# Kernel tuning notes

Hardware: AMD Instinct MI355X
Metric: run time of the kernel (lower is better)

## Reference

```python
import jax, jax.numpy as jnp
import numpy as np

DIM = 128; NH = 4; WS = 7; SS = 3
ZP, HP, WP = 14, 56, 56
NMLP = 512; EPS = 1e-5
N = WS ** 3  # tokens per window (343)


def _ln(x, g, b):
    m = x.mean(-1, keepdims=True)
    v = x.var(-1, keepdims=True)
    return (x - m) / jnp.sqrt(v + EPS) * g + b


def _rel_index():
    # static relative-position index for a cubic (WS,WS,WS) window
    c = np.stack(np.meshgrid(np.arange(WS), np.arange(WS), np.arange(WS), indexing='ij')).reshape(3, -1)
    rel = (c[:, :, None] - c[:, None, :]).transpose(1, 2, 0) + (WS - 1)
    rel[..., 0] *= (2 * WS - 1) ** 2
    rel[..., 1] *= (2 * WS - 1)
    return rel.sum(-1).reshape(-1)  # [N*N]


def _attn_mask():
    # static shifted-window attention mask, [nW, N, N]
    img = np.zeros((ZP, HP, WP), np.float32)
    cnt = 0
    sl = (slice(0, -WS), slice(-WS, -SS), slice(-SS, None))
    for z in sl:
        for h in sl:
            for w in sl:
                img[z, h, w] = cnt
                cnt += 1
    m = img.reshape(ZP // WS, WS, HP // WS, WS, WP // WS, WS)
    m = m.transpose(0, 2, 4, 1, 3, 5).reshape(-1, N)
    d = m[:, None, :] - m[:, :, None]
    return np.where(d != 0, np.float32(-100.0), np.float32(0.0))


_REL_IDX = jnp.asarray(_rel_index())
_MASK = jnp.asarray(_attn_mask())


def setup_inputs() -> dict:
    key = jax.random.key(0)
    ks = jax.random.split(key, 8)
    return {
        'x': jax.random.normal(ks[0], (2, ZP, HP, WP, DIM), jnp.float32),
        'norm1_g': jnp.ones((DIM,), jnp.float32),
        'norm1_b': jnp.zeros((DIM,), jnp.float32),
        'qkv_w': jax.random.normal(ks[1], (DIM, 3 * DIM), jnp.float32) * 0.02,
        'qkv_b': jnp.zeros((3 * DIM,), jnp.float32),
        'rel_table': jax.random.normal(ks[2], ((2 * WS - 1) ** 3, NH), jnp.float32) * 0.02,
        'proj_w': jax.random.normal(ks[3], (DIM, DIM), jnp.float32) * 0.02,
        'proj_b': jnp.zeros((DIM,), jnp.float32),
        'norm2_g': jnp.ones((DIM,), jnp.float32),
        'norm2_b': jnp.zeros((DIM,), jnp.float32),
        'fc1_w': jax.random.normal(ks[4], (DIM, NMLP), jnp.float32) * 0.02,
        'fc1_b': jnp.zeros((NMLP,), jnp.float32),
        'fc2_w': jax.random.normal(ks[5], (NMLP, DIM), jnp.float32) * 0.02,
        'fc2_b': jnp.zeros((DIM,), jnp.float32),
    }


def reference(x, norm1_g, norm1_b, qkv_w, qkv_b, rel_table, proj_w, proj_b,
              norm2_g, norm2_b, fc1_w, fc1_b, fc2_w, fc2_b):
    B, Z, H, W, C = x.shape
    hd = C // NH
    scale = hd ** -0.5
    shortcut = x
    xn = _ln(x, norm1_g, norm1_b)
    # cyclic shift
    xs = jnp.roll(xn, (-SS, -SS, -SS), axis=(1, 2, 3))
    # window partition -> [B*nW, N, C]
    xw = xs.reshape(B, Z // WS, WS, H // WS, WS, W // WS, WS, C)
    xw = xw.transpose(0, 1, 3, 5, 2, 4, 6, 7).reshape(-1, N, C)
    qkv = (xw @ qkv_w + qkv_b).reshape(-1, N, 3, NH, hd).transpose(2, 0, 3, 1, 4)
    q, k, v = qkv[0], qkv[1], qkv[2]  # [Bn, NH, N, hd]
    attn = jnp.einsum('bhnd,bhmd->bhnm', q * scale, k)
    bias = rel_table[_REL_IDX].reshape(N, N, NH).transpose(2, 0, 1)  # [NH, N, N]
    attn = attn + bias[None]
    nW = _MASK.shape[0]
    attn = attn.reshape(B, nW, NH, N, N) + _MASK[None, :, None]
    attn = jax.nn.softmax(attn.reshape(-1, NH, N, N), axis=-1)
    out = jnp.einsum('bhnm,bhmd->bhnd', attn, v)
    out = out.transpose(0, 2, 1, 3).reshape(-1, N, C)
    out = out @ proj_w + proj_b
    # window reverse -> [B, Z, H, W, C]
    out = out.reshape(B, Z // WS, H // WS, W // WS, WS, WS, WS, C)
    out = out.transpose(0, 1, 4, 2, 5, 3, 6, 7).reshape(B, Z, H, W, C)
    out = jnp.roll(out, (SS, SS, SS), axis=(1, 2, 3))
    x1 = shortcut + out
    y = _ln(x1, norm2_g, norm2_b)
    y = jax.nn.gelu(y @ fc1_w + fc1_b, approximate=False) @ fc2_w + fc2_b
    return x1 + y
```

## Files before the change

### kernel.cpp

```cpp
#include <hip/hip_runtime.h>


typedef __attribute__((ext_vector_type(8))) _Float16 half8;
typedef __attribute__((ext_vector_type(4))) _Float16 half4;
typedef __attribute__((ext_vector_type(4))) float floatx4;

#define DEV static __device__ __forceinline__

DEV floatx4 MFMA(half8 a, half8 b, floatx4 c) {
  return __builtin_amdgcn_mfma_f32_16x16x32_f16(a, b, c, 0, 0, 0);
}

DEV float gelu_f(float v) {
  return v / (1.f + __expf(-1.702f * v));
}

DEV void f4arr(float4 v, float o[4]) {
  o[0] = v.x; o[1] = v.y; o[2] = v.z; o[3] = v.w;
}

DEV void stage_load(half8 pf[8], const _Float16* src, int rst, int tid) {
#pragma unroll
  for (int it = 0; it < 8; ++it) {
    int e = it * 256 + tid;
    int row = e >> 4, seg = e & 15;
    pf[it] = *(const half8*)&src[(size_t)row * rst + seg * 8];
  }
}
DEV void stage_store(_Float16* wb, const half8 pf[8], int tid) {
#pragma unroll
  for (int it = 0; it < 8; ++it) {
    int e = it * 256 + tid;
    int row = e >> 4, seg = e & 15;
    *(half8*)&wb[row * 136 + seg * 8] = pf[it];
  }
}
DEV void stage_tile(_Float16* wb, const _Float16* src, int rst, int tid) {
  half8 pf[8];
  stage_load(pf, src, rst, tid);
  stage_store(wb, pf, tid);
}

__global__ __launch_bounds__(256) void k_prep(
    const float* __restrict__ rel, _Float16* __restrict__ biasH,
    const float* __restrict__ w1, const float* __restrict__ w2,
    const float* __restrict__ wq, const float* __restrict__ wp,
    _Float16* __restrict__ w1h, _Float16* __restrict__ w2h,
    _Float16* __restrict__ wqh, _Float16* __restrict__ wph) {
  int gid = blockIdx.x * 256 + threadIdx.x;
  if (gid < 495616) {
    int reg = gid & 3, ml = (gid >> 2) & 15;
    int t = gid >> 6;
    int rb = t % 88; t /= 88;
    int nt = t % 22; int h = t / 22;
    int row = rb * 4 + reg, col = nt * 16 + ml;
    float val = -30000.f;
    if (row < 343 && col < 343) {
      int lzi = row / 49, ri = row - lzi * 49, lhi = ri / 7, lwi = ri - lhi * 7;
      int lzj = col / 49, rj = col - lzj * 49, lhj = rj / 7, lwj = rj - lhj * 7;
      int idx = (lzi - lzj + 6) * 169 + (lhi - lhj + 6) * 13 + (lwi - lwj + 6);
      val = rel[idx * 4 + h];
    }
    biasH[gid] = (_Float16)val;
    return;
  }
  int i = gid - 495616;
  if (i < 65536) {
    int n = i >> 7, k = i & 127;
    w1h[i] = (_Float16)w1[k * 512 + n];
  } else if (i < 131072) {
    int j = i - 65536; int n = j >> 9, k = j & 511;
    w2h[j] = (_Float16)w2[k * 128 + n];
  } else if (i < 180224) {
    int j = i - 131072; int n = j >> 7, k = j & 127;
    wqh[j] = (_Float16)wq[k * 384 + n];
  } else if (i < 196608) {
    int j = i - 180224; int n = j >> 7, k = j & 127;
    wph[j] = (_Float16)wp[k * 128 + n];
  }
}

__global__ __launch_bounds__(256) void k_ln_qkv(
    const float* __restrict__ x, const float* __restrict__ g1,
    const float* __restrict__ b1, const _Float16* __restrict__ wqh,
    const float* __restrict__ bq, _Float16* __restrict__ qkv) {
  __shared__ __align__(16) _Float16 wb[128 * 136];
  const int tid = threadIdx.x, lane = tid & 63, wid = tid >> 6;
  const int ml = lane & 15, quad = lane >> 4;
  const int task = blockIdx.x * 4 + wid;
  const int w = task / 11, pr = task - (task / 11) * 11;
  const int b_ = w >> 7, r = w & 127;
  const int wz = r >> 6, wh = (r >> 3) & 7, ww = r & 7;

  half8 a0[4], a1[4];
#pragma unroll
  for (int hf = 0; hf < 2; ++hf) {
    int t = pr * 32 + hf * 16 + ml; if (t > 342) t = 342;
    int lz = t / 49, rr = t - lz * 49, lh = rr / 7, lw = rr - lh * 7;
    int oz = wz * 7 + lz + 3; if (oz >= 14) oz -= 14;
    int oh = wh * 7 + lh + 3; if (oh >= 56) oh -= 56;
    int ow = ww * 7 + lw + 3; if (ow >= 56) ow -= 56;
    const float* xp = x + ((((b_ * 14 + oz) * 56 + oh) * 56 + ow) << 7);
    float xv[32];
    float s = 0.f, ss = 0.f;
#pragma unroll
    for (int ks = 0; ks < 4; ++ks) {
      float4 p0 = *(const float4*)(xp + ks * 32 + quad * 8);
      float4 p1 = *(const float4*)(xp + ks * 32 + quad * 8 + 4);
      xv[ks * 8 + 0] = p0.x; xv[ks * 8 + 1] = p0.y; xv[ks * 8 + 2] = p0.z; xv[ks * 8 + 3] = p0.w;
      xv[ks * 8 + 4] = p1.x; xv[ks * 8 + 5] = p1.y; xv[ks * 8 + 6] = p1.z; xv[ks * 8 + 7] = p1.w;
      s += (p0.x + p0.y) + (p0.z + p0.w) + (p1.x + p1.y) + (p1.z + p1.w);
      ss += (p0.x * p0.x + p0.y * p0.y) + (p0.z * p0.z + p0.w * p0.w) +
            (p1.x * p1.x + p1.y * p1.y) + (p1.z * p1.z + p1.w * p1.w);
    }
    s += __shfl_xor(s, 16); s += __shfl_xor(s, 32);
    ss += __shfl_xor(ss, 16); ss += __shfl_xor(ss, 32);
    float mean = s * 0.0078125f;
    float rstd = rsqrtf(ss * 0.0078125f - mean * mean + 1e-5f);
#pragma unroll
    for (int ks = 0; ks < 4; ++ks) {
      int k0 = ks * 32 + quad * 8;
      float4 gg0 = *(const float4*)(g1 + k0), gg1 = *(const float4*)(g1 + k0 + 4);
      float4 bb0 = *(const float4*)(b1 + k0), bb1 = *(const float4*)(b1 + k0 + 4);
      half8 a;
      a[0] = (_Float16)((xv[ks * 8 + 0] - mean) * rstd * gg0.x + bb0.x);
      a[1] = (_Float16)((xv[ks * 8 + 1] - mean) * rstd * gg0.y + bb0.y);
      a[2] = (_Float16)((xv[ks * 8 + 2] - mean) * rstd * gg0.z + bb0.z);
      a[3] = (_Float16)((xv[ks * 8 + 3] - mean) * rstd * gg0.w + bb0.w);
      a[4] = (_Float16)((xv[ks * 8 + 4] - mean) * rstd * gg1.x + bb1.x);
      a[5] = (_Float16)((xv[ks * 8 + 5] - mean) * rstd * gg1.y + bb1.y);
      a[6] = (_Float16)((xv[ks * 8 + 6] - mean) * rstd * gg1.z + bb1.z);
      a[7] = (_Float16)((xv[ks * 8 + 7] - mean) * rstd * gg1.w + bb1.w);
      if (hf == 0) a0[ks] = a; else a1[ks] = a;
    }
  }

  const int t0 = pr * 32 + ml;
  const int t1 = t0 + 16;
  _Float16* q0 = qkv + ((size_t)w * 343 + t0) * 384;
  _Float16* q1 = qkv + ((size_t)w * 343 + (t1 < 343 ? t1 : 342)) * 384;

  for (int c = 0; c < 3; ++c) {
    __syncthreads();
    stage_tile(wb, wqh + (size_t)c * 128 * 128, 128, tid);
    __syncthreads();
    for (int ntl = 0; ntl < 8; ++ntl) {
      floatx4 acc0 = {0.f, 0.f, 0.f, 0.f}, acc1 = {0.f, 0.f, 0.f, 0.f};
#pragma unroll
      for (int ks = 0; ks < 4; ++ks) {
        half8 bb = *(const half8*)&wb[(ntl * 16 + ml) * 136 + ks * 32 + quad * 8];
        acc0 = MFMA(bb, a0[ks], acc0);
        acc1 = MFMA(bb, a1[ks], acc1);
      }
      const int colb = c * 128 + ntl * 16 + quad * 4;
      float qb[4]; f4arr(*(const float4*)&bq[colb], qb);
      half4 s0, s1;
#pragma unroll
      for (int reg = 0; reg < 4; ++reg) {
        s0[reg] = (_Float16)(acc0[reg] + qb[reg]);
        s1[reg] = (_Float16)(acc1[reg] + qb[reg]);
      }
      *(half4*)&q0[colb] = s0;
      if (t1 < 343) *(half4*)&q1[colb] = s1;
    }
  }
}

__global__ __launch_bounds__(512, 2) void k_attn(const _Float16* __restrict__ qkv,
                                                 const _Float16* __restrict__ biasH,
                                                 _Float16* __restrict__ aout) {
  __shared__ __align__(16) _Float16 kl[352 * 40];
  __shared__ __align__(16) _Float16 vt[32 * 360];
  __shared__ __align__(16) _Float16 P[8][16 * 360];
  __shared__ float sums[8][16];
  __shared__ unsigned char region[352];
  const int tid = threadIdx.x;
  const int w = blockIdx.x >> 2, head = blockIdx.x & 3;
  const int r = w & 127;
  const int wz = r >> 6, wh = (r >> 3) & 7, ww = r & 7;
  const bool fz = (wz == 1), fh = (wh == 7), fw = (ww == 7);

  for (int t = tid; t < 352; t += 512) {
    int rg = 255;
    if (t < 343) {
      int lz = t / 49, rr = t - lz * 49, lh = rr / 7, lw = rr - lh * 7;
      int rz = fz ? (lz < 4 ? 1 : 2) : 0;
      int rh2 = fh ? (lh < 4 ? 1 : 2) : 0;
      int rw2 = fw ? (lw < 4 ? 1 : 2) : 0;
      rg = rz * 9 + rh2 * 3 + rw2;
    }
    region[t] = (unsigned char)rg;
  }
  const _Float16* qkvw = qkv + (size_t)w * 343 * 384;
  for (int e = tid; e < 352 * 4; e += 512) {
    int t = e >> 2, d8 = (e & 3) * 8;
    half8 v;
    if (t < 343) {
      v = *(const half8*)&qkvw[t * 384 + 128 + head * 32 + d8];
    } else {
#pragma unroll
      for (int j = 0; j < 8; ++j) v[j] = (_Float16)0.f;
    }
    *(half8*)&kl[t * 40 + d8] = v;
  }
  for (int e = tid; e < 343 * 4; e += 512) {
    int t = e >> 2, d8 = (e & 3) * 8;
    half8 v = *(const half8*)&qkvw[t * 384 + 256 + head * 32 + d8];
#pragma unroll
    for (int j = 0; j < 8; ++j) vt[(d8 + j) * 360 + t] = v[j];
  }
  for (int e = tid; e < 9 * 32; e += 512) {
    int t = 343 + (e >> 5), d = e & 31;
    vt[d * 360 + t] = (_Float16)0.f;
  }
  __syncthreads();

  const int lane = tid & 63, wid = tid >> 6;
  const int ml = lane & 15, quad = lane >> 4;
  _Float16* Pw = &P[wid][0];
  const float scale = 0.17677669529663687f;

  for (int rt = wid; rt < 22; rt += 8) {
    const int row0 = rt * 16;
    int qrow = row0 + ml; if (qrow > 342) qrow = 342;
    half8 aq = *(const half8*)&qkvw[qrow * 384 + head * 32 + quad * 8];
    floatx4 S[22];
#pragma unroll
    for (int nt = 0; nt < 22; ++nt) {
      half8 bk = *(const half8*)&kl[(nt * 16 + ml) * 40 + quad * 8];
      S[nt] = MFMA(aq, bk, (floatx4){0.f, 0.f, 0.f, 0.f});
    }
    int rrow[4];
#pragma unroll
    for (int reg = 0; reg < 4; ++reg) rrow[reg] = region[row0 + quad * 4 + reg];
    const int rb = rt * 4 + quad;
    float sm[4] = {0.f, 0.f, 0.f, 0.f};
#pragma unroll
    for (int nt = 0; nt < 22; ++nt) {
      half4 b4 = *(const half4*)&biasH[((((head * 22 + nt) * 88 + rb) << 4) + ml) * 4];
      int rc = region[nt * 16 + ml];
#pragma unroll
      for (int reg = 0; reg < 4; ++reg) {
        float v = fmaf(S[nt][reg], scale, (float)b4[reg]);
        if (rc != rrow[reg]) v = -30000.f;
        float e = __expf(v);
        sm[reg] += e;
        Pw[(quad * 4 + reg) * 360 + nt * 16 + ml] = (_Float16)e;
      }
    }
#pragma unroll
    for (int d = 1; d < 16; d <<= 1)
#pragma unroll
      for (int reg = 0; reg < 4; ++reg) sm[reg] += __shfl_xor(sm[reg], d, 16);
    if (ml == 0) {
#pragma unroll
      for (int reg = 0; reg < 4; ++reg) sums[wid][quad * 4 + reg] = sm[reg];
    }
    floatx4 o0 = {0.f, 0.f, 0.f, 0.f}, o1 = {0.f, 0.f, 0.f, 0.f};
#pragma unroll
    for (int ks = 0; ks < 11; ++ks) {
      half8 bp = *(const half8*)&Pw[ml * 360 + ks * 32 + quad * 8];
      half8 a0 = *(const half8*)&vt[ml * 360 + ks * 32 + quad * 8];
      half8 a1 = *(const half8*)&vt[(16 + ml) * 360 + ks * 32 + quad * 8];
      o0 = MFMA(a0, bp, o0);
      o1 = MFMA(a1, bp, o1);
    }
    const int orow = row0 + ml;
    if (orow < 343) {
      float inv = 1.f / sums[wid][ml];
      _Float16* op = aout + ((size_t)w * 343 + orow) * 128 + head * 32;
      half4 s0, s1;
#pragma unroll
      for (int reg = 0; reg < 4; ++reg) {
        s0[reg] = (_Float16)(o0[reg] * inv);
        s1[reg] = (_Float16)(o1[reg] * inv);
      }
      *(half4*)&op[quad * 4] = s0;
      *(half4*)&op[16 + quad * 4] = s1;
    }
  }
}

__global__ __launch_bounds__(256, 2) void k_pm(
    const _Float16* __restrict__ aout, const _Float16* __restrict__ wph,
    const float* __restrict__ bp, const float* __restrict__ x,
    const float* __restrict__ g2, const float* __restrict__ nb2,
    const _Float16* __restrict__ w1h, const float* __restrict__ bfc1,
    const _Float16* __restrict__ w2h, const float* __restrict__ bfc2,
    float* __restrict__ out) {
  __shared__ __align__(16) _Float16 hc[4][32 * 136];
  __shared__ __align__(16) _Float16 wb[128 * 136];
  const int tid = threadIdx.x, lane = tid & 63, wid = tid >> 6;
  const int ml = lane & 15, quad = lane >> 4;
  const int task = blockIdx.x * 4 + wid;
  const int w = task / 11, pr = task - (task / 11) * 11;
  const int b_ = w >> 7, r = w & 127;
  const int wz = r >> 6, wh = (r >> 3) & 7, ww = r & 7;
  const _Float16* ap = aout + (size_t)w * 343 * 128;
  _Float16* hw = &hc[wid][0];

  half8 pf[8];
  stage_load(pf, wph, 128, tid);

  int ra = pr * 32 + ml; if (ra > 342) ra = 342;
  int rbm = pr * 32 + 16 + ml; if (rbm > 342) rbm = 342;
  half8 a0[4], a1[4];
#pragma unroll
  for (int ks = 0; ks < 4; ++ks) {
    a0[ks] = *(const half8*)&ap[ra * 128 + ks * 32 + quad * 8];
    a1[ks] = *(const half8*)&ap[rbm * 128 + ks * 32 + quad * 8];
  }
  int tok[2];
#pragma unroll
  for (int mt = 0; mt < 2; ++mt) {
    int t = pr * 32 + mt * 16 + ml;
    if (t < 343) {
      int lz = t / 49, rr = t - lz * 49, lh = rr / 7, lw = rr - lh * 7;
      int oz = wz * 7 + lz + 3; if (oz >= 14) oz -= 14;
      int oh = wh * 7 + lh + 3; if (oh >= 56) oh -= 56;
      int ow = ww * 7 + lw + 3; if (ow >= 56) ow -= 56;
      tok[mt] = ((b_ * 14 + oz) * 56 + oh) * 56 + ow;
    } else {
      tok[mt] = -1;
    }
  }
  stage_store(wb, pf, tid);
  __syncthreads();
  stage_load(pf, w1h, 128, tid);

  floatx4 px[8][2];
  for (int nt = 0; nt < 8; ++nt) {
    floatx4 acc0 = {0.f, 0.f, 0.f, 0.f}, acc1 = {0.f, 0.f, 0.f, 0.f};
#pragma unroll
    for (int ks = 0; ks < 4; ++ks) {
      half8 bb = *(const half8*)&wb[(nt * 16 + ml) * 136 + ks * 32 + quad * 8];
      acc0 = MFMA(bb, a0[ks], acc0);
      acc1 = MFMA(bb, a1[ks], acc1);
    }
    const int colb = nt * 16 + quad * 4;
    float pb4[4]; f4arr(*(const float4*)&bp[colb], pb4);
    float xr0[4] = {0.f, 0.f, 0.f, 0.f}, xr1[4] = {0.f, 0.f, 0.f, 0.f};
    if (tok[0] >= 0) f4arr(*(const float4*)&x[(size_t)tok[0] * 128 + colb], xr0);
    if (tok[1] >= 0) f4arr(*(const float4*)&x[(size_t)tok[1] * 128 + colb], xr1);
#pragma unroll
    for (int reg = 0; reg < 4; ++reg) {
      px[nt][0][reg] = acc0[reg] + pb4[reg] + xr0[reg];
      px[nt][1][reg] = acc1[reg] + pb4[reg] + xr1[reg];
    }
  }

  float mean[2], rstd[2];
#pragma unroll
  for (int mt = 0; mt < 2; ++mt) {
    float s = 0.f, ss = 0.f;
#pragma unroll
    for (int nt = 0; nt < 8; ++nt)
#pragma unroll
      for (int reg = 0; reg < 4; ++reg) {
        float v = px[nt][mt][reg];
        s += v; ss += v * v;
      }
    s += __shfl_xor(s, 16); s += __shfl_xor(s, 32);
    ss += __shfl_xor(ss, 16); ss += __shfl_xor(ss, 32);
    float m = s * 0.0078125f;
    mean[mt] = m;
    rstd[mt] = rsqrtf(ss * 0.0078125f - m * m + 1e-5f);
  }

  for (int nt = 0; nt < 8; ++nt) {
    const int colb = nt * 16 + quad * 4;
    float g4[4], nb4[4];
    f4arr(*(const float4*)&g2[colb], g4);
    f4arr(*(const float4*)&nb2[colb], nb4);
#pragma unroll
    for (int mt = 0; mt < 2; ++mt) {
      half4 h;
#pragma unroll
      for (int reg = 0; reg < 4; ++reg)
        h[reg] = (_Float16)((px[nt][mt][reg] - mean[mt]) * rstd[mt] * g4[reg] + nb4[reg]);
      *(half4*)&hw[(mt * 16 + ml) * 136 + colb] = h;
    }
  }
  half8 ay[2][4];
#pragma unroll
  for (int mt = 0; mt < 2; ++mt)
#pragma unroll
    for (int ks = 0; ks < 4; ++ks)
      ay[mt][ks] = *(const half8*)&hw[(mt * 16 + ml) * 136 + ks * 32 + quad * 8];

  floatx4 acc2[8][2];
#pragma unroll
  for (int nt = 0; nt < 8; ++nt)
#pragma unroll
    for (int mt = 0; mt < 2; ++mt) acc2[nt][mt] = (floatx4){0.f, 0.f, 0.f, 0.f};

  for (int ch = 0; ch < 4; ++ch) {
    __syncthreads();
    stage_store(wb, pf, tid);
    __syncthreads();
    stage_load(pf, w2h + (size_t)ch * 128, 512, tid);
    for (int nt = 0; nt < 8; ++nt) {
      floatx4 f0 = {0.f, 0.f, 0.f, 0.f}, f1 = {0.f, 0.f, 0.f, 0.f};
#pragma unroll
      for (int ks = 0; ks < 4; ++ks) {
        half8 bb = *(const half8*)&wb[(nt * 16 + ml) * 136 + ks * 32 + quad * 8];
        f0 = MFMA(bb, ay[0][ks], f0);
        f1 = MFMA(bb, ay[1][ks], f1);
      }
      const int colb = nt * 16 + quad * 4;
      float fb4[4]; f4arr(*(const float4*)&bfc1[ch * 128 + colb], fb4);
      half4 h0, h1;
#pragma unroll
      for (int reg = 0; reg < 4; ++reg) {
        h0[reg] = (_Float16)gelu_f(f0[reg] + fb4[reg]);
        h1[reg] = (_Float16)gelu_f(f1[reg] + fb4[reg]);
      }
      *(half4*)&hw[ml * 136 + colb] = h0;
      *(half4*)&hw[(16 + ml) * 136 + colb] = h1;
    }
    __syncthreads();
    stage_store(wb, pf, tid);
    __syncthreads();
    if (ch < 3) stage_load(pf, w1h + (size_t)(ch + 1) * 128 * 128, 128, tid);
#pragma unroll
    for (int ks = 0; ks < 4; ++ks) {
      half8 A0 = *(const half8*)&hw[ml * 136 + ks * 32 + quad * 8];
      half8 A1 = *(const half8*)&hw[(16 + ml) * 136 + ks * 32 + quad * 8];
#pragma unroll
      for (int nt = 0; nt < 8; ++nt) {
        half8 bb = *(const half8*)&wb[(nt * 16 + ml) * 136 + ks * 32 + quad * 8];
        acc2[nt][0] = MFMA(bb, A0, acc2[nt][0]);
        acc2[nt][1] = MFMA(bb, A1, acc2[nt][1]);
      }
    }
  }

  for (int nt = 0; nt < 8; ++nt) {
    const int colb = nt * 16 + quad * 4;
    float fb4[4]; f4arr(*(const float4*)&bfc2[colb], fb4);
#pragma unroll
    for (int mt = 0; mt < 2; ++mt) {
      if (tok[mt] >= 0) {
        float4 o;
        o.x = px[nt][mt][0] + acc2[nt][mt][0] + fb4[0];
        o.y = px[nt][mt][1] + acc2[nt][mt][1] + fb4[1];
        o.z = px[nt][mt][2] + acc2[nt][mt][2] + fb4[2];
        o.w = px[nt][mt][3] + acc2[nt][mt][3] + fb4[3];
        *(float4*)&out[(size_t)tok[mt] * 128 + colb] = o;
      }
    }
  }
}

extern "C" void kernel_launch(void* const* d_in, const int* in_sizes, int n_in,
                              void* d_out, int out_size, void* d_ws, size_t ws_size,
                              hipStream_t stream) {
  (void)in_sizes; (void)n_in; (void)out_size; (void)ws_size;
  const float* x   = (const float*)d_in[0];
  const float* g1  = (const float*)d_in[1];
  const float* b1  = (const float*)d_in[2];
  const float* wq  = (const float*)d_in[3];
  const float* bq  = (const float*)d_in[4];
  const float* rel = (const float*)d_in[5];
  const float* wp  = (const float*)d_in[6];
  const float* bp  = (const float*)d_in[7];
  const float* g2  = (const float*)d_in[8];
  const float* b2_ = (const float*)d_in[9];
  const float* w1  = (const float*)d_in[10];
  const float* bf1 = (const float*)d_in[11];
  const float* w2  = (const float*)d_in[12];
  const float* bf2 = (const float*)d_in[13];

  char* ws = (char*)d_ws;
  _Float16* qkv   = (_Float16*)(ws);
  _Float16* aout  = (_Float16*)(ws + 67436544);
  _Float16* biasH = (_Float16*)(ws + 89915392);
  _Float16* w1h   = (_Float16*)(ws + 91897856);
  _Float16* w2h   = (_Float16*)(ws + 92028928);
  _Float16* wqh   = (_Float16*)(ws + 92160000);
  _Float16* wph   = (_Float16*)(ws + 92258304);
  float*    out   = (float*)d_out;

  hipLaunchKernelGGL(k_prep,   dim3(2704), dim3(256), 0, stream,
                     rel, biasH, w1, w2, wq, wp, w1h, w2h, wqh, wph);
  hipLaunchKernelGGL(k_ln_qkv, dim3(704),  dim3(256), 0, stream, x, g1, b1, wqh, bq, qkv);
  hipLaunchKernelGGL(k_attn,   dim3(1024), dim3(512), 0, stream, qkv, biasH, aout);
  hipLaunchKernelGGL(k_pm,     dim3(704),  dim3(256), 0, stream,
                     aout, wph, bp, x, g2, b2_, w1h, bf1, w2h, bf2, out);
}
```

Measured before the change: 288.5 us.

## Keep softmax probabilities in registers and feed PV MFMA directly, dropping LDS P buffer

The QK^T product is transposed (K as the A operand, Q as B) so each lane holds a column slice of scores matching the B-operand layout of a 16x16x16 MFMA. The exponentiated probabilities then stay in registers and feed the PV product directly, removing the per-wave P scratch in shared memory and the sums array. The bias table layout is reordered to match the new fragment mapping. Freeing about 90KB of LDS lets launch bounds go up to 4 blocks per CU, at the cost of more register pressure from holding 22 half4 fragments and using the smaller-K MFMA instruction.

```diff
diff --git a/kernel.cpp b/kernel.cpp
--- a/kernel.cpp
+++ b/kernel.cpp
@@ -9,6 +9,9 @@
 
 DEV floatx4 MFMA(half8 a, half8 b, floatx4 c) {
   return __builtin_amdgcn_mfma_f32_16x16x32_f16(a, b, c, 0, 0, 0);
+}
+DEV floatx4 MFMA16(half4 a, half4 b, floatx4 c) {
+  return __builtin_amdgcn_mfma_f32_16x16x16f16(a, b, c, 0, 0, 0);
 }
 
 DEV float gelu_f(float v) {
@@ -49,15 +52,15 @@
     _Float16* __restrict__ wqh, _Float16* __restrict__ wph) {
   int gid = blockIdx.x * 256 + threadIdx.x;
   if (gid < 495616) {
-    int reg = gid & 3, ml = (gid >> 2) & 15;
-    int t = gid >> 6;
-    int rb = t % 88; t /= 88;
+    int reg = gid & 3, quad = (gid >> 2) & 3, ml = (gid >> 4) & 15;
+    int t = gid >> 8;
+    int rt = t % 22; t /= 22;
     int nt = t % 22; int h = t / 22;
-    int row = rb * 4 + reg, col = nt * 16 + ml;
+    int q = rt * 16 + ml, kv = nt * 16 + quad * 4 + reg;
     float val = -30000.f;
-    if (row < 343 && col < 343) {
-      int lzi = row / 49, ri = row - lzi * 49, lhi = ri / 7, lwi = ri - lhi * 7;
-      int lzj = col / 49, rj = col - lzj * 49, lhj = rj / 7, lwj = rj - lhj * 7;
+    if (q < 343 && kv < 343) {
+      int lzi = q / 49, ri = q - lzi * 49, lhi = ri / 7, lwi = ri - lhi * 7;
+      int lzj = kv / 49, rj = kv - lzj * 49, lhj = rj / 7, lwj = rj - lhj * 7;
       int idx = (lzi - lzj + 6) * 169 + (lhi - lhj + 6) * 13 + (lwi - lwj + 6);
       val = rel[idx * 4 + h];
     }
@@ -166,14 +169,12 @@
   }
 }
 
-__global__ __launch_bounds__(512, 2) void k_attn(const _Float16* __restrict__ qkv,
+__global__ __launch_bounds__(512, 4) void k_attn(const _Float16* __restrict__ qkv,
                                                  const _Float16* __restrict__ biasH,
                                                  _Float16* __restrict__ aout) {
   __shared__ __align__(16) _Float16 kl[352 * 40];
-  __shared__ __align__(16) _Float16 vt[32 * 360];
-  __shared__ __align__(16) _Float16 P[8][16 * 360];
-  __shared__ float sums[8][16];
-  __shared__ unsigned char region[352];
+  __shared__ __align__(16) _Float16 vt[32 * 364];
+  __shared__ __align__(4) unsigned char region[352];
   const int tid = threadIdx.x;
   const int w = blockIdx.x >> 2, head = blockIdx.x & 3;
   const int r = w & 127;
@@ -207,67 +208,68 @@
     int t = e >> 2, d8 = (e & 3) * 8;
     half8 v = *(const half8*)&qkvw[t * 384 + 256 + head * 32 + d8];
 #pragma unroll
-    for (int j = 0; j < 8; ++j) vt[(d8 + j) * 360 + t] = v[j];
+    for (int j = 0; j < 8; ++j) vt[(d8 + j) * 364 + t] = v[j];
   }
   for (int e = tid; e < 9 * 32; e += 512) {
     int t = 343 + (e >> 5), d = e & 31;
-    vt[d * 360 + t] = (_Float16)0.f;
+    vt[d * 364 + t] = (_Float16)0.f;
   }
   __syncthreads();
 
   const int lane = tid & 63, wid = tid >> 6;
   const int ml = lane & 15, quad = lane >> 4;
-  _Float16* Pw = &P[wid][0];
   const float scale = 0.17677669529663687f;
 
   for (int rt = wid; rt < 22; rt += 8) {
     const int row0 = rt * 16;
     int qrow = row0 + ml; if (qrow > 342) qrow = 342;
-    half8 aq = *(const half8*)&qkvw[qrow * 384 + head * 32 + quad * 8];
-    floatx4 S[22];
+    half8 bq8 = *(const half8*)&qkvw[qrow * 384 + head * 32 + quad * 8];
+    const int rq = region[qrow];
+    const int bbase = (head * 484 + rt) * 256 + ml * 16 + quad * 4;
+
+    half4 p4[22];
+    float sm = 0.f;
+#pragma unroll
+    for (int h2 = 0; h2 < 2; ++h2) {
+      floatx4 S[11];
+#pragma unroll
+      for (int k2 = 0; k2 < 11; ++k2) {
+        int nt = h2 * 11 + k2;
+        half8 ak = *(const half8*)&kl[(nt * 16 + ml) * 40 + quad * 8];
+        S[k2] = MFMA(ak, bq8, (floatx4){0.f, 0.f, 0.f, 0.f});
+      }
+#pragma unroll
+      for (int k2 = 0; k2 < 11; ++k2) {
+        int nt = h2 * 11 + k2;
+        half4 b4 = *(const half4*)&biasH[bbase + nt * 5632];
+        uchar4 rc = *(const uchar4*)&region[nt * 16 + quad * 4];
+        unsigned char rca[4] = {rc.x, rc.y, rc.z, rc.w};
+        half4 p;
+#pragma unroll
+        for (int reg = 0; reg < 4; ++reg) {
+          float v = fmaf(S[k2][reg], scale, (float)b4[reg]);
+          if (rca[reg] != rq) v = -30000.f;
+          float e = __expf(v);
+          sm += e;
+          p[reg] = (_Float16)e;
+        }
+        p4[nt] = p;
+      }
+    }
+    sm += __shfl_xor(sm, 16);
+    sm += __shfl_xor(sm, 32);
+
+    floatx4 o0 = {0.f, 0.f, 0.f, 0.f}, o1 = {0.f, 0.f, 0.f, 0.f};
 #pragma unroll
     for (int nt = 0; nt < 22; ++nt) {
-      half8 bk = *(const half8*)&kl[(nt * 16 + ml) * 40 + quad * 8];
-      S[nt] = MFMA(aq, bk, (floatx4){0.f, 0.f, 0.f, 0.f});
-    }
-    int rrow[4];
-#pragma unroll
-    for (int reg = 0; reg < 4; ++reg) rrow[reg] = region[row0 + quad * 4 + reg];
-    const int rb = rt * 4 + quad;
-    float sm[4] = {0.f, 0.f, 0.f, 0.f};
-#pragma unroll
-    for (int nt = 0; nt < 22; ++nt) {
-      half4 b4 = *(const half4*)&biasH[((((head * 22 + nt) * 88 + rb) << 4) + ml) * 4];
-      int rc = region[nt * 16 + ml];
-#pragma unroll
-      for (int reg = 0; reg < 4; ++reg) {
-        float v = fmaf(S[nt][reg], scale, (float)b4[reg]);
-        if (rc != rrow[reg]) v = -30000.f;
-        float e = __expf(v);
-        sm[reg] += e;
-        Pw[(quad * 4 + reg) * 360 + nt * 16 + ml] = (_Float16)e;
-      }
-    }
-#pragma unroll
-    for (int d = 1; d < 16; d <<= 1)
-#pragma unroll
-      for (int reg = 0; reg < 4; ++reg) sm[reg] += __shfl_xor(sm[reg], d, 16);
-    if (ml == 0) {
-#pragma unroll
-      for (int reg = 0; reg < 4; ++reg) sums[wid][quad * 4 + reg] = sm[reg];
-    }
-    floatx4 o0 = {0.f, 0.f, 0.f, 0.f}, o1 = {0.f, 0.f, 0.f, 0.f};
-#pragma unroll
-    for (int ks = 0; ks < 11; ++ks) {
-      half8 bp = *(const half8*)&Pw[ml * 360 + ks * 32 + quad * 8];
-      half8 a0 = *(const half8*)&vt[ml * 360 + ks * 32 + quad * 8];
-      half8 a1 = *(const half8*)&vt[(16 + ml) * 360 + ks * 32 + quad * 8];
-      o0 = MFMA(a0, bp, o0);
-      o1 = MFMA(a1, bp, o1);
+      half4 a0 = *(const half4*)&vt[ml * 364 + nt * 16 + quad * 4];
+      half4 a1 = *(const half4*)&vt[(16 + ml) * 364 + nt * 16 + quad * 4];
+      o0 = MFMA16(a0, p4[nt], o0);
+      o1 = MFMA16(a1, p4[nt], o1);
     }
     const int orow = row0 + ml;
     if (orow < 343) {
-      float inv = 1.f / sums[wid][ml];
+      float inv = 1.f / sm;
       _Float16* op = aout + ((size_t)w * 343 + orow) * 128 + head * 32;
       half4 s0, s1;
 #pragma unroll
```

New measurement: 472.9 us. +63.9%, slower.
